# Kernel optimization log

Hardware: AMD Instinct MI355X
Metric: run time of the kernel (lower is better)

Reference implementation:

```python
import jax, jax.numpy as jnp
import numpy as np

N_NODES = 50000
N_EDGES = 600000
F_IN = 128
H_DIM = 256
N_CLASSES = 16
N_GRAPHS = 64


def _sage_conv(x, edge_index, W_l, W_r, b, num_nodes):
    # PyG SAGEConv (aggr='mean', root_weight=True):
    #   out = lin_l(mean_{j in N(i)} x_j) + lin_r(x_i)
    src, dst = edge_index[0], edge_index[1]
    msg_sum = jax.ops.segment_sum(x[src], dst, num_segments=num_nodes)      # [N, F]
    cnt = jax.ops.segment_sum(jnp.ones((edge_index.shape[1],), x.dtype), dst,
                              num_segments=num_nodes)                        # [N]
    mean = msg_sum / jnp.maximum(cnt, 1.0)[:, None]
    return mean @ W_l + x @ W_r + b


def _global_mean_pool(x, batch, num_graphs):
    s = jax.ops.segment_sum(x, batch, num_segments=num_graphs)               # [G, C]
    c = jax.ops.segment_sum(jnp.ones((x.shape[0],), x.dtype), batch,
                            num_segments=num_graphs)                         # [G]
    return s / jnp.maximum(c, 1.0)[:, None]


def setup_inputs() -> dict:
    key = jax.random.key(0)
    ks = jax.random.split(key, 9)
    x = jax.random.normal(ks[0], (N_NODES, F_IN), dtype=jnp.float32)
    edge_index = jax.random.randint(ks[1], (2, N_EDGES), 0, N_NODES)
    batch = jnp.sort(jax.random.randint(ks[2], (N_NODES,), 0, N_GRAPHS))
    # SAGEConv params (glorot-ish scale)
    def w(k, fi, fo):
        return jax.random.normal(k, (fi, fo), dtype=jnp.float32) / np.sqrt(fi)
    return {
        "x": x,
        "edge_index": edge_index,
        "batch": batch,
        "W1_l": w(ks[3], F_IN, H_DIM),
        "W1_r": w(ks[4], F_IN, H_DIM),
        "b1": jnp.zeros((H_DIM,), jnp.float32),
        "W2_l": w(ks[5], H_DIM, N_CLASSES),
        "W2_r": w(ks[6], H_DIM, N_CLASSES),
        "b2": jnp.zeros((N_CLASSES,), jnp.float32),
    }


def reference(x, edge_index, batch, W1_l, W1_r, b1, W2_l, W2_r, b2):
    n = x.shape[0]
    h = _sage_conv(x, edge_index, W1_l, W1_r, b1, n)
    h = jax.nn.relu(h)
    h = _sage_conv(h, edge_index, W2_l, W2_r, b2, n)
    h = jax.nn.relu(h)
    g = _global_mean_pool(h, batch, N_GRAPHS)
    return jax.nn.log_softmax(g, axis=1)
```

## Files before the change

### kernel.cpp

```cpp
#include <hip/hip_runtime.h>

#define N_NODES   50000
#define N_EDGES   600000
#define F_IN      128
#define H_DIM     256
#define N_CLASSES 16
#define N_GRAPHS  64
#define M_PAD     50048

typedef unsigned short ushort_t;
typedef unsigned int   uint_t;
typedef __attribute__((ext_vector_type(8))) short bf16x8;
typedef __attribute__((ext_vector_type(4))) float f32x4;

__device__ inline ushort_t f2bf(float f) {
    union { float f; uint_t u; } v; v.f = f;
    uint_t r = v.u + 0x7FFF + ((v.u >> 16) & 1);
    return (ushort_t)(r >> 16);
}
__device__ inline float bf2f(uint_t u) {
    union { uint_t u; float f; } v; v.u = u << 16;
    return v.f;
}
__device__ inline void load_lds16(const void* g, void* l) {
    __builtin_amdgcn_global_load_lds(
        (const __attribute__((address_space(1))) void*)g,
        (__attribute__((address_space(3))) void*)l, 16, 0, 0);
}

__global__ void zero_kernel(uint_t* __restrict__ w, int n) {
    int i = blockIdx.x * blockDim.x + threadIdx.x;
    if (i < n) w[i] = 0u;
}

__global__ void hist_kernel(const int* __restrict__ dst, int* __restrict__ deg) {
    int e = blockIdx.x * blockDim.x + threadIdx.x;
    if (e < N_EDGES) atomicAdd(&deg[dst[e]], 1);
}

__global__ __launch_bounds__(256) void scan1_kernel(const int* __restrict__ deg,
                                                    int* __restrict__ bsum) {
    __shared__ int sc[256];
    const int t = threadIdx.x;
    const int i = blockIdx.x * 256 + t;
    sc[t] = (i < N_NODES) ? deg[i] : 0;
    __syncthreads();
    for (int s = 128; s > 0; s >>= 1) {
        if (t < s) sc[t] += sc[t + s];
        __syncthreads();
    }
    if (t == 0) bsum[blockIdx.x] = sc[0];
}

__global__ __launch_bounds__(256) void scan2_kernel(int* __restrict__ bsum, int nb) {
    __shared__ int sc[256];
    const int t = threadIdx.x;
    const int v = (t < nb) ? bsum[t] : 0;
    sc[t] = v;
    __syncthreads();
    for (int s = 1; s < 256; s <<= 1) {
        int add = (t >= s) ? sc[t - s] : 0;
        __syncthreads();
        sc[t] += add;
        __syncthreads();
    }
    if (t < nb) bsum[t] = sc[t] - v;
}

__global__ __launch_bounds__(256) void scan3_kernel(const int* __restrict__ deg,
                                                    const int* __restrict__ bsum,
                                                    int* __restrict__ off,
                                                    int* __restrict__ cursor) {
    __shared__ int sc[256];
    const int t = threadIdx.x;
    const int i = blockIdx.x * 256 + t;
    const int d = (i < N_NODES) ? deg[i] : 0;
    sc[t] = d;
    __syncthreads();
    for (int s = 1; s < 256; s <<= 1) {
        int add = (t >= s) ? sc[t - s] : 0;
        __syncthreads();
        sc[t] += add;
        __syncthreads();
    }
    if (i < N_NODES) {
        const int o = bsum[blockIdx.x] + sc[t] - d;
        off[i] = o;
        cursor[i] = o;
    }
    if (i == N_NODES) off[i] = N_EDGES;
}

__global__ void scatter_ids_kernel(const int* __restrict__ src,
                                   const int* __restrict__ dst,
                                   int* __restrict__ cursor,
                                   int* __restrict__ ssrc) {
    int e = blockIdx.x * blockDim.x + threadIdx.x;
    if (e >= N_EDGES) return;
    int pos = atomicAdd(&cursor[dst[e]], 1);
    ssrc[pos] = src[e];
}

__global__ void xcopy_kernel(const float* __restrict__ x, ushort_t* __restrict__ ha) {
    int t = blockIdx.x * blockDim.x + threadIdx.x;
    if (t >= N_NODES * 32) return;
    int n = t >> 5, c = t & 31;
    const float4 v = *reinterpret_cast<const float4*>(x + (size_t)n * F_IN + c * 4);
    uint2 pk;
    pk.x = (uint_t)f2bf(v.x) | ((uint_t)f2bf(v.y) << 16);
    pk.y = (uint_t)f2bf(v.z) | ((uint_t)f2bf(v.w) << 16);
    *reinterpret_cast<uint2*>(ha + (size_t)n * 256 + 128 + c * 4) = pk;
}

__global__ __launch_bounds__(256) void agg1_kernel(const int* __restrict__ off,
                                                   const int* __restrict__ ssrc,
                                                   ushort_t* __restrict__ ha,
                                                   float* __restrict__ invdeg) {
    const int n = blockIdx.x * 4 + (threadIdx.x >> 6);
    if (n >= N_NODES) return;
    const int lane = threadIdx.x & 63;
    const int slot = lane >> 4;
    const int c    = lane & 15;
    const int o0 = off[n], o1 = off[n + 1];
    float a[8] = {0.f, 0.f, 0.f, 0.f, 0.f, 0.f, 0.f, 0.f};
    for (int e = o0 + slot; e < o1; e += 4) {
        const int s = ssrc[e];
        const uint4 v = *reinterpret_cast<const uint4*>(ha + (size_t)s * 256 + 128 + c * 8);
        a[0] += bf2f(v.x & 0xFFFFu); a[1] += bf2f(v.x >> 16);
        a[2] += bf2f(v.y & 0xFFFFu); a[3] += bf2f(v.y >> 16);
        a[4] += bf2f(v.z & 0xFFFFu); a[5] += bf2f(v.z >> 16);
        a[6] += bf2f(v.w & 0xFFFFu); a[7] += bf2f(v.w >> 16);
    }
#pragma unroll
    for (int i = 0; i < 8; ++i) {
        a[i] += __shfl_xor(a[i], 16);
        a[i] += __shfl_xor(a[i], 32);
    }
    const float iv = 1.0f / fmaxf((float)(o1 - o0), 1.0f);
    if (slot == 0) {
        uint4 pk;
        pk.x = (uint_t)f2bf(a[0] * iv) | ((uint_t)f2bf(a[1] * iv) << 16);
        pk.y = (uint_t)f2bf(a[2] * iv) | ((uint_t)f2bf(a[3] * iv) << 16);
        pk.z = (uint_t)f2bf(a[4] * iv) | ((uint_t)f2bf(a[5] * iv) << 16);
        pk.w = (uint_t)f2bf(a[6] * iv) | ((uint_t)f2bf(a[7] * iv) << 16);
        *reinterpret_cast<uint4*>(ha + (size_t)n * 256 + c * 8) = pk;
        if (c == 0) invdeg[n] = iv;
    }
}

__global__ __launch_bounds__(256) void btprep_kernel(
    const float* __restrict__ W1l, const float* __restrict__ W1r,
    const float* __restrict__ W2l, const float* __restrict__ W2r,
    ushort_t* __restrict__ Bt, ushort_t* __restrict__ Bt2) {
    const int bi = blockIdx.x;
    const int k = threadIdx.x;
    if (bi < 256) {
        const float v = (k < 128) ? W1l[k * H_DIM + bi] : W1r[(k - 128) * H_DIM + bi];
        Bt[bi * 256 + k] = f2bf(v);
    } else {
        const int c = bi - 256;
        const float v = (c < 16) ? W2l[k * N_CLASSES + c] : W2r[k * N_CLASSES + (c - 16)];
        Bt2[c * 256 + k] = f2bf(v);
    }
}

__global__ __launch_bounds__(256) void gemm1_fused_kernel(
    const ushort_t* __restrict__ ha, const ushort_t* __restrict__ Bt,
    const ushort_t* __restrict__ Bt2, const float* __restrict__ b1,
    float* __restrict__ p, float* __restrict__ r) {
    __shared__ ushort_t sA[64 * 256];
    __shared__ ushort_t sB[64 * 256];
    const int tid  = threadIdx.x;
    const int mblk = blockIdx.x;

    const char* gA = (const char*)ha + (size_t)mblk * 32768;
    const char* gB = (const char*)Bt;
#pragma unroll
    for (int i = 0; i < 8; ++i) {
        const int d = (i * 256 + tid) * 16;
        const int s = d ^ (((d >> 9) & 7) << 4);
        load_lds16(gA + s, (char*)sA + (d & ~1023));
    }
#pragma unroll
    for (int i = 0; i < 8; ++i) {
        const int d = (i * 256 + tid) * 16;
        const int s = d ^ (((d >> 9) & 7) << 4);
        load_lds16(gB + s, (char*)sB + (d & ~1023));
    }
    __syncthreads();

    const int w    = tid >> 6;
    const int lane = tid & 63;
    const int lr   = lane & 15;
    const int hi   = lane >> 4;
    const int m0   = w * 16;

    bf16x8 afr[8];
    {
        const int row = m0 + lr;
        const int sw = (row & 7) << 4;
#pragma unroll
        for (int ks = 0; ks < 8; ++ks)
            afr[ks] = *reinterpret_cast<const bf16x8*>(
                (const char*)sA + ((row * 512 + ks * 64 + hi * 16) ^ sw));
    }

    f32x4 acc[16];
#pragma unroll
    for (int t = 0; t < 16; ++t) acc[t] = (f32x4){0.f, 0.f, 0.f, 0.f};

#pragma unroll
    for (int ph = 0; ph < 4; ++ph) {
#pragma unroll
        for (int fnl = 0; fnl < 4; ++fnl) {
            const int rn = fnl * 16 + lr;
            const int sw = (rn & 7) << 4;
#pragma unroll
            for (int ks = 0; ks < 8; ++ks) {
                const bf16x8 bfr = *reinterpret_cast<const bf16x8*>(
                    (const char*)sB + ((rn * 512 + ks * 64 + hi * 16) ^ sw));
                acc[ph * 4 + fnl] = __builtin_amdgcn_mfma_f32_16x16x32_bf16(
                    afr[ks], bfr, acc[ph * 4 + fnl], 0, 0, 0);
            }
        }
        __syncthreads();
        if (ph < 3) {
#pragma unroll
            for (int i = 0; i < 8; ++i) {
                const int d = (i * 256 + tid) * 16;
                const int s = d ^ (((d >> 9) & 7) << 4);
                load_lds16(gB + (ph + 1) * 32768 + s, (char*)sB + (d & ~1023));
            }
            __syncthreads();
        }
    }

#pragma unroll
    for (int t = 0; t < 16; ++t) {
        const int colG = t * 16 + lr;
        const float bias = b1[colG];
#pragma unroll
        for (int i = 0; i < 4; ++i) {
            const int row = m0 + hi * 4 + i;
            const float h = fmaxf(acc[t][i] + bias, 0.f);
            const int ad = (row * 512 + colG * 2) ^ ((row & 7) << 4);
            *reinterpret_cast<ushort_t*>((char*)sB + ad) = f2bf(h);
        }
    }
    __syncthreads();

    const char* bt2b = (const char*)Bt2;
    const int nr = m0 + lr;
    const int swn = (nr & 7) << 4;
    f32x4 acc2[2] = {(f32x4){0.f, 0.f, 0.f, 0.f}, (f32x4){0.f, 0.f, 0.f, 0.f}};
#pragma unroll
    for (int fc = 0; fc < 2; ++fc) {
#pragma unroll
        for (int k2 = 0; k2 < 8; ++k2) {
            const bf16x8 a2 = *reinterpret_cast<const bf16x8*>(
                bt2b + (fc * 16 + lr) * 512 + k2 * 64 + hi * 16);
            const bf16x8 b2 = *reinterpret_cast<const bf16x8*>(
                (const char*)sB + ((nr * 512 + k2 * 64 + hi * 16) ^ swn));
            acc2[fc] = __builtin_amdgcn_mfma_f32_16x16x32_bf16(a2, b2, acc2[fc], 0, 0, 0);
        }
    }

    const int node = mblk * 64 + nr;
    if (node < N_NODES) {
#pragma unroll
        for (int i = 0; i < 4; ++i) {
            p[(size_t)node * N_CLASSES + hi * 4 + i] = acc2[0][i];
            r[(size_t)node * N_CLASSES + hi * 4 + i] = acc2[1][i];
        }
    }
}

__global__ __launch_bounds__(256) void agg2_kernel(const float* __restrict__ p,
                                                   const int* __restrict__ off,
                                                   const int* __restrict__ ssrc,
                                                   float* __restrict__ psum) {
    const int n = blockIdx.x * 4 + (threadIdx.x >> 6);
    if (n >= N_NODES) return;
    const int lane = threadIdx.x & 63;
    const int slot = lane >> 2;
    const int c    = lane & 3;
    const int o0 = off[n], o1 = off[n + 1];
    float4 acc = {0.f, 0.f, 0.f, 0.f};
    for (int e = o0 + slot; e < o1; e += 16) {
        const int s = ssrc[e];
        const float4 v = *reinterpret_cast<const float4*>(p + (size_t)s * N_CLASSES + c * 4);
        acc.x += v.x; acc.y += v.y; acc.z += v.z; acc.w += v.w;
    }
#pragma unroll
    for (int o = 4; o < 64; o <<= 1) {
        acc.x += __shfl_xor(acc.x, o);
        acc.y += __shfl_xor(acc.y, o);
        acc.z += __shfl_xor(acc.z, o);
        acc.w += __shfl_xor(acc.w, o);
    }
    if (slot == 0)
        *reinterpret_cast<float4*>(psum + (size_t)n * N_CLASSES + c * 4) = acc;
}

__global__ __launch_bounds__(256) void pool_kernel(
    const float* __restrict__ psum, const float* __restrict__ r,
    const float* __restrict__ invdeg, const float* __restrict__ b2,
    const int* __restrict__ batch,
    float* __restrict__ gsum, float* __restrict__ gcnt) {
    __shared__ float lgsum[N_GRAPHS * N_CLASSES];
    __shared__ float lgcnt[N_GRAPHS];
    __shared__ int gminmax[2];
    const int t = threadIdx.x;
    const int base = blockIdx.x * 64;
#pragma unroll
    for (int k = 0; k < 4; ++k) lgsum[t + 256 * k] = 0.f;
    if (t < N_GRAPHS) lgcnt[t] = 0.f;
    if (t == 0) {
        gminmax[0] = batch[base];
        int last = base + 63; if (last >= N_NODES) last = N_NODES - 1;
        gminmax[1] = batch[last];
    }
    __syncthreads();

    const int j = t & 15;
    const float bj = b2[j];
#pragma unroll
    for (int k = 0; k < 4; ++k) {
        const int i = base + (t >> 4) + 16 * k;
        if (i < N_NODES) {
            float h = psum[(size_t)i * N_CLASSES + j] * invdeg[i]
                      + r[(size_t)i * N_CLASSES + j] + bj;
            h = fmaxf(h, 0.f);
            const int g = batch[i];
            atomicAdd(&lgsum[g * N_CLASSES + j], h);
            if (j == 0) atomicAdd(&lgcnt[g], 1.0f);
        }
    }
    __syncthreads();

    const int gmin = gminmax[0], gmax = gminmax[1];
    for (int gg = gmin + (t >> 4); gg <= gmax; gg += 16) {
        const float v = lgsum[gg * N_CLASSES + j];
        if (v != 0.f) atomicAdd(&gsum[gg * N_CLASSES + j], v);
    }
    if (t < N_GRAPHS) {
        const int gg = gmin + t;
        if (gg <= gmax) {
            const float c = lgcnt[gg];
            if (c != 0.f) atomicAdd(&gcnt[gg], c);
        }
    }
}

__global__ void lsm_kernel(const float* __restrict__ gsum,
                           const float* __restrict__ gcnt,
                           float* __restrict__ out) {
    int g = threadIdx.x;
    if (g >= N_GRAPHS) return;
    const float iv = 1.0f / fmaxf(gcnt[g], 1.0f);
    float v[N_CLASSES];
    float m = -1e30f;
#pragma unroll
    for (int j = 0; j < N_CLASSES; ++j) {
        v[j] = gsum[g * N_CLASSES + j] * iv;
        m = fmaxf(m, v[j]);
    }
    float s = 0.f;
#pragma unroll
    for (int j = 0; j < N_CLASSES; ++j) s += expf(v[j] - m);
    const float lse = logf(s);
#pragma unroll
    for (int j = 0; j < N_CLASSES; ++j) out[g * N_CLASSES + j] = v[j] - m - lse;
}

extern "C" void kernel_launch(void* const* d_in, const int* in_sizes, int n_in,
                              void* d_out, int out_size, void* d_ws, size_t ws_size,
                              hipStream_t stream) {
    const float* x    = (const float*)d_in[0];
    const int*   ei   = (const int*)d_in[1];
    const int*   batch= (const int*)d_in[2];
    const float* W1l  = (const float*)d_in[3];
    const float* W1r  = (const float*)d_in[4];
    const float* b1   = (const float*)d_in[5];
    const float* W2l  = (const float*)d_in[6];
    const float* W2r  = (const float*)d_in[7];
    const float* b2   = (const float*)d_in[8];
    float* out = (float*)d_out;

    const int* src = ei;
    const int* dst = ei + N_EDGES;

    float* ws     = (float*)d_ws;
    int*   deg    = (int*)ws;
    float* invdeg = ws;
    float* gsum   = ws + 50000;
    float* gcnt   = gsum + 1024;
    int*   off    = (int*)(gcnt + 64);
    int*   cursor = off + 50004;
    int*   ssrc   = cursor + 50000;
    int*   bsum   = ssrc + 600000;
    ushort_t* Bt  = (ushort_t*)(bsum + 256);
    ushort_t* Bt2 = Bt + 65536;
    ushort_t* ha  = Bt2 + 8192;
    float* p      = (float*)(ha + (size_t)M_PAD * 256);
    float* r      = p + 800000;
    float* psum   = (float*)ha;

    const int zero_elems = 50000 + 1024 + 64;
    zero_kernel<<<(zero_elems + 255) / 256, 256, 0, stream>>>((uint_t*)ws, zero_elems);

    const int NB = (N_NODES + 255) / 256;
    hist_kernel<<<(N_EDGES + 255) / 256, 256, 0, stream>>>(dst, deg);
    scan1_kernel<<<NB, 256, 0, stream>>>(deg, bsum);
    scan2_kernel<<<1, 256, 0, stream>>>(bsum, NB);
    scan3_kernel<<<NB, 256, 0, stream>>>(deg, bsum, off, cursor);
    scatter_ids_kernel<<<(N_EDGES + 255) / 256, 256, 0, stream>>>(src, dst, cursor, ssrc);
    xcopy_kernel<<<(N_NODES * 32 + 255) / 256, 256, 0, stream>>>(x, ha);
    agg1_kernel<<<(N_NODES + 3) / 4, 256, 0, stream>>>(off, ssrc, ha, invdeg);
    btprep_kernel<<<288, 256, 0, stream>>>(W1l, W1r, W2l, W2r, Bt, Bt2);
    gemm1_fused_kernel<<<M_PAD / 64, 256, 0, stream>>>(ha, Bt, Bt2, b1, p, r);
    agg2_kernel<<<(N_NODES + 3) / 4, 256, 0, stream>>>(p, off, ssrc, psum);
    pool_kernel<<<(N_NODES + 63) / 64, 256, 0, stream>>>(psum, r, invdeg, b2, batch, gsum, gcnt);
    lsm_kernel<<<1, 64, 0, stream>>>(gsum, gcnt, out);
}
```

Baseline: 171.1 us.

## Fuse workspace zeroing into xcopy, widen agg1 lanes, halve GEMM B tile

The separate zero kernel is removed and its work folded into xcopy, which now launches first, saving one launch. agg1 now has each lane load two 16-byte chunks per edge with 8 edge slots per node, giving more memory parallelism per wavefront at the cost of one extra shuffle stage. The GEMM's B staging buffer is halved to 32 rows and iterated over 8 phases, with the layer-2 input written into sA instead, cutting LDS use to allow higher occupancy but adding more barriers.

New measurement: 166.5 us. 2.7% less time.

```diff
diff --git a/kernel.cpp b/kernel.cpp
--- a/kernel.cpp
+++ b/kernel.cpp
@@ -7,6 +7,7 @@
 #define N_CLASSES 16
 #define N_GRAPHS  64
 #define M_PAD     50048
+#define ZERO_WORDS (50000 + 1024 + 64)
 
 typedef unsigned short ushort_t;
 typedef unsigned int   uint_t;
@@ -26,11 +27,6 @@
     __builtin_amdgcn_global_load_lds(
         (const __attribute__((address_space(1))) void*)g,
         (__attribute__((address_space(3))) void*)l, 16, 0, 0);
-}
-
-__global__ void zero_kernel(uint_t* __restrict__ w, int n) {
-    int i = blockIdx.x * blockDim.x + threadIdx.x;
-    if (i < n) w[i] = 0u;
 }
 
 __global__ void hist_kernel(const int* __restrict__ dst, int* __restrict__ deg) {
@@ -101,8 +97,10 @@
     ssrc[pos] = src[e];
 }
 
-__global__ void xcopy_kernel(const float* __restrict__ x, ushort_t* __restrict__ ha) {
+__global__ void xcopy_kernel(const float* __restrict__ x, ushort_t* __restrict__ ha,
+                             uint_t* __restrict__ wszero) {
     int t = blockIdx.x * blockDim.x + threadIdx.x;
+    if (t < ZERO_WORDS) wszero[t] = 0u;
     if (t >= N_NODES * 32) return;
     int n = t >> 5, c = t & 31;
     const float4 v = *reinterpret_cast<const float4*>(x + (size_t)n * F_IN + c * 4);
@@ -119,31 +117,46 @@
     const int n = blockIdx.x * 4 + (threadIdx.x >> 6);
     if (n >= N_NODES) return;
     const int lane = threadIdx.x & 63;
-    const int slot = lane >> 4;
-    const int c    = lane & 15;
+    const int slot = lane >> 3;
+    const int c    = lane & 7;
     const int o0 = off[n], o1 = off[n + 1];
-    float a[8] = {0.f, 0.f, 0.f, 0.f, 0.f, 0.f, 0.f, 0.f};
-    for (int e = o0 + slot; e < o1; e += 4) {
+    float a[16];
+#pragma unroll
+    for (int i = 0; i < 16; ++i) a[i] = 0.f;
+    for (int e = o0 + slot; e < o1; e += 8) {
         const int s = ssrc[e];
-        const uint4 v = *reinterpret_cast<const uint4*>(ha + (size_t)s * 256 + 128 + c * 8);
-        a[0] += bf2f(v.x & 0xFFFFu); a[1] += bf2f(v.x >> 16);
-        a[2] += bf2f(v.y & 0xFFFFu); a[3] += bf2f(v.y >> 16);
-        a[4] += bf2f(v.z & 0xFFFFu); a[5] += bf2f(v.z >> 16);
-        a[6] += bf2f(v.w & 0xFFFFu); a[7] += bf2f(v.w >> 16);
-    }
-#pragma unroll
-    for (int i = 0; i < 8; ++i) {
+        const ushort_t* row = ha + (size_t)s * 256 + 128;
+        const uint4 v0 = *reinterpret_cast<const uint4*>(row + c * 8);
+        const uint4 v1 = *reinterpret_cast<const uint4*>(row + 64 + c * 8);
+        a[0] += bf2f(v0.x & 0xFFFFu); a[1] += bf2f(v0.x >> 16);
+        a[2] += bf2f(v0.y & 0xFFFFu); a[3] += bf2f(v0.y >> 16);
+        a[4] += bf2f(v0.z & 0xFFFFu); a[5] += bf2f(v0.z >> 16);
+        a[6] += bf2f(v0.w & 0xFFFFu); a[7] += bf2f(v0.w >> 16);
+        a[8]  += bf2f(v1.x & 0xFFFFu); a[9]  += bf2f(v1.x >> 16);
+        a[10] += bf2f(v1.y & 0xFFFFu); a[11] += bf2f(v1.y >> 16);
+        a[12] += bf2f(v1.z & 0xFFFFu); a[13] += bf2f(v1.z >> 16);
+        a[14] += bf2f(v1.w & 0xFFFFu); a[15] += bf2f(v1.w >> 16);
+    }
+#pragma unroll
+    for (int i = 0; i < 16; ++i) {
+        a[i] += __shfl_xor(a[i], 8);
         a[i] += __shfl_xor(a[i], 16);
         a[i] += __shfl_xor(a[i], 32);
     }
     const float iv = 1.0f / fmaxf((float)(o1 - o0), 1.0f);
     if (slot == 0) {
-        uint4 pk;
-        pk.x = (uint_t)f2bf(a[0] * iv) | ((uint_t)f2bf(a[1] * iv) << 16);
-        pk.y = (uint_t)f2bf(a[2] * iv) | ((uint_t)f2bf(a[3] * iv) << 16);
-        pk.z = (uint_t)f2bf(a[4] * iv) | ((uint_t)f2bf(a[5] * iv) << 16);
-        pk.w = (uint_t)f2bf(a[6] * iv) | ((uint_t)f2bf(a[7] * iv) << 16);
-        *reinterpret_cast<uint4*>(ha + (size_t)n * 256 + c * 8) = pk;
+        uint4 pk0, pk1;
+        pk0.x = (uint_t)f2bf(a[0] * iv) | ((uint_t)f2bf(a[1] * iv) << 16);
+        pk0.y = (uint_t)f2bf(a[2] * iv) | ((uint_t)f2bf(a[3] * iv) << 16);
+        pk0.z = (uint_t)f2bf(a[4] * iv) | ((uint_t)f2bf(a[5] * iv) << 16);
+        pk0.w = (uint_t)f2bf(a[6] * iv) | ((uint_t)f2bf(a[7] * iv) << 16);
+        pk1.x = (uint_t)f2bf(a[8]  * iv) | ((uint_t)f2bf(a[9]  * iv) << 16);
+        pk1.y = (uint_t)f2bf(a[10] * iv) | ((uint_t)f2bf(a[11] * iv) << 16);
+        pk1.z = (uint_t)f2bf(a[12] * iv) | ((uint_t)f2bf(a[13] * iv) << 16);
+        pk1.w = (uint_t)f2bf(a[14] * iv) | ((uint_t)f2bf(a[15] * iv) << 16);
+        ushort_t* orow = ha + (size_t)n * 256;
+        *reinterpret_cast<uint4*>(orow + c * 8) = pk0;
+        *reinterpret_cast<uint4*>(orow + 64 + c * 8) = pk1;
         if (c == 0) invdeg[n] = iv;
     }
 }
@@ -169,7 +182,7 @@
     const ushort_t* __restrict__ Bt2, const float* __restrict__ b1,
     float* __restrict__ p, float* __restrict__ r) {
     __shared__ ushort_t sA[64 * 256];
-    __shared__ ushort_t sB[64 * 256];
+    __shared__ ushort_t sB[32 * 256];
     const int tid  = threadIdx.x;
     const int mblk = blockIdx.x;
 
@@ -182,7 +195,7 @@
         load_lds16(gA + s, (char*)sA + (d & ~1023));
     }
 #pragma unroll
-    for (int i = 0; i < 8; ++i) {
+    for (int i = 0; i < 4; ++i) {
         const int d = (i * 256 + tid) * 16;
         const int s = d ^ (((d >> 9) & 7) << 4);
         load_lds16(gB + s, (char*)sB + (d & ~1023));
@@ -210,26 +223,26 @@
     for (int t = 0; t < 16; ++t) acc[t] = (f32x4){0.f, 0.f, 0.f, 0.f};
 
 #pragma unroll
-    for (int ph = 0; ph < 4; ++ph) {
-#pragma unroll
-        for (int fnl = 0; fnl < 4; ++fnl) {
+    for (int ph = 0; ph < 8; ++ph) {
+#pragma unroll
+        for (int fnl = 0; fnl < 2; ++fnl) {
             const int rn = fnl * 16 + lr;
             const int sw = (rn & 7) << 4;
 #pragma unroll
             for (int ks = 0; ks < 8; ++ks) {
                 const bf16x8 bfr = *reinterpret_cast<const bf16x8*>(
                     (const char*)sB + ((rn * 512 + ks * 64 + hi * 16) ^ sw));
-                acc[ph * 4 + fnl] = __builtin_amdgcn_mfma_f32_16x16x32_bf16(
-                    afr[ks], bfr, acc[ph * 4 + fnl], 0, 0, 0);
+                acc[ph * 2 + fnl] = __builtin_amdgcn_mfma_f32_16x16x32_bf16(
+                    afr[ks], bfr, acc[ph * 2 + fnl], 0, 0, 0);
             }
         }
         __syncthreads();
-        if (ph < 3) {
-#pragma unroll
-            for (int i = 0; i < 8; ++i) {
+        if (ph < 7) {
+#pragma unroll
+            for (int i = 0; i < 4; ++i) {
                 const int d = (i * 256 + tid) * 16;
                 const int s = d ^ (((d >> 9) & 7) << 4);
-                load_lds16(gB + (ph + 1) * 32768 + s, (char*)sB + (d & ~1023));
+                load_lds16(gB + (ph + 1) * 16384 + s, (char*)sB + (d & ~1023));
             }
             __syncthreads();
         }
@@ -244,7 +257,7 @@
             const int row = m0 + hi * 4 + i;
             const float h = fmaxf(acc[t][i] + bias, 0.f);
             const int ad = (row * 512 + colG * 2) ^ ((row & 7) << 4);
-            *reinterpret_cast<ushort_t*>((char*)sB + ad) = f2bf(h);
+            *reinterpret_cast<ushort_t*>((char*)sA + ad) = f2bf(h);
         }
     }
     __syncthreads();
@@ -260,7 +273,7 @@
             const bf16x8 a2 = *reinterpret_cast<const bf16x8*>(
                 bt2b + (fc * 16 + lr) * 512 + k2 * 64 + hi * 16);
             const bf16x8 b2 = *reinterpret_cast<const bf16x8*>(
-                (const char*)sB + ((nr * 512 + k2 * 64 + hi * 16) ^ swn));
+                (const char*)sA + ((nr * 512 + k2 * 64 + hi * 16) ^ swn));
             acc2[fc] = __builtin_amdgcn_mfma_f32_16x16x32_bf16(a2, b2, acc2[fc], 0, 0, 0);
         }
     }
@@ -406,16 +419,13 @@
     float* r      = p + 800000;
     float* psum   = (float*)ha;
 
-    const int zero_elems = 50000 + 1024 + 64;
-    zero_kernel<<<(zero_elems + 255) / 256, 256, 0, stream>>>((uint_t*)ws, zero_elems);
-
     const int NB = (N_NODES + 255) / 256;
+    xcopy_kernel<<<(N_NODES * 32 + 255) / 256, 256, 0, stream>>>(x, ha, (uint_t*)ws);
     hist_kernel<<<(N_EDGES + 255) / 256, 256, 0, stream>>>(dst, deg);
     scan1_kernel<<<NB, 256, 0, stream>>>(deg, bsum);
     scan2_kernel<<<1, 256, 0, stream>>>(bsum, NB);
     scan3_kernel<<<NB, 256, 0, stream>>>(deg, bsum, off, cursor);
     scatter_ids_kernel<<<(N_EDGES + 255) / 256, 256, 0, stream>>>(src, dst, cursor, ssrc);
-    xcopy_kernel<<<(N_NODES * 32 + 255) / 256, 256, 0, stream>>>(x, ha);
     agg1_kernel<<<(N_NODES + 3) / 4, 256, 0, stream>>>(off, ssrc, ha, invdeg);
     btprep_kernel<<<288, 256, 0, stream>>>(W1l, W1r, W2l, W2r, Bt, Bt2);
     gemm1_fused_kernel<<<M_PAD / 64, 256, 0, stream>>>(ha, Bt, Bt2, b1, p, r);
```
